# Performance work log

Measured on AMD Instinct MI355X. Metric: run time of the kernel, lower is better.

Reference implementation:

```python
import jax, jax.numpy as jnp
import numpy as np

B, S, D = 16, 8192, 256  # batch, seq_len, feature dim (== hdims)
HDIMS, HEADS = 256, 8
NEG_BIG = 1e12


def setup_inputs() -> dict:
    key = jax.random.key(0)
    k1, k2, k3 = jax.random.split(key, 3)
    x = jax.random.normal(k1, (B, S, D), dtype=jnp.float32)
    mask = jnp.ones((B, S), dtype=jnp.bool_)
    # glorot-ish scaling for stability
    k_kernel = jax.random.normal(k2, (D, HDIMS), dtype=jnp.float32) * (1.0 / np.sqrt(D))
    o_kernel = jax.random.normal(k3, (HDIMS, HEADS), dtype=jnp.float32) * (1.0 / np.sqrt(HDIMS))
    return {"x": x, "mask": mask, "k_kernel": k_kernel, "o_kernel": o_kernel}


def reference(x, mask, k_kernel, o_kernel):
    # scores: Dense(tanh) -> Dense(heads), shape (B, S, HEADS)
    w = jnp.tanh(x @ k_kernel) @ o_kernel
    m = mask.astype(jnp.float32)[..., None]            # (B, S, 1)
    w = w - (1.0 - m) * NEG_BIG
    w = jax.nn.softmax(w, axis=1)                      # softmax over sequence
    # fused weighted-sum pooling: avoids (B,S,H,D) broadcast intermediate
    pooled = jnp.einsum('bsh,bsd->bhd', w, x)          # (B, HEADS, D)
    return pooled.reshape(x.shape[0], HEADS * HDIMS)   # (B, HEADS*HDIMS)
```

## Files before the change

kernel.cpp:

```cpp
#include <hip/hip_runtime.h>

#define S_LEN 8192
#define DIM   256
#define CHUNK 512
#define TB    64
#define NIT   8
#define NBLK  256

typedef __attribute__((ext_vector_type(8))) short          short8;
typedef __attribute__((ext_vector_type(4))) unsigned short u16x4;
typedef __attribute__((ext_vector_type(4))) unsigned int   u32x4;
typedef __attribute__((ext_vector_type(4))) float          f32x4;
typedef __attribute__((ext_vector_type(8))) __bf16         bf16x8;

static __device__ __forceinline__ unsigned short f2bf(float f){
  return __builtin_bit_cast(unsigned short, (__bf16)f);
}
static __device__ __forceinline__ unsigned pk2bf(float lo, float hi){
  return (unsigned)f2bf(lo) | ((unsigned)f2bf(hi) << 16);
}
static __device__ __forceinline__ float bf2f(unsigned short h){
  unsigned int u = ((unsigned int)h) << 16;
  return __builtin_bit_cast(float, u);
}
static __device__ __forceinline__ float fast_tanh(float x){
  float e = __expf(2.0f * x);
  return 1.0f - 2.0f / (e + 1.0f);
}
static __device__ __forceinline__ f32x4 mfma_bf16(short8 a, short8 b, f32x4 c){
  return __builtin_amdgcn_mfma_f32_16x16x32_bf16(
      __builtin_bit_cast(bf16x8, a), __builtin_bit_cast(bf16x8, b), c, 0, 0, 0);
}
static __device__ __forceinline__ void softbar(){
  asm volatile("s_waitcnt lgkmcnt(0)\n\ts_barrier" ::: "memory");
}

__global__ void k_prep(const float* __restrict__ kk, unsigned short* __restrict__ KT){
  int idx = blockIdx.x * 512 + threadIdx.x;
  int n = idx >> 8, k = idx & 255;
  KT[(n << 8) + k] = f2bf(kk[(k << 8) + n]);
}


__global__ __launch_bounds__(512, 2) void k_main(
    const float* __restrict__ x, const int* __restrict__ mask,
    const float* __restrict__ ok, const unsigned short* __restrict__ KT,
    float* __restrict__ ACC, float* __restrict__ ML)
{
  __shared__ __align__(16) unsigned char sXB [32768];
  __shared__ __align__(16) unsigned char sXT2[65536];
  __shared__ __align__(16) unsigned char sT2 [32768];
  __shared__ __align__(16) unsigned char sOT [16*528];
  __shared__ __align__(16) unsigned char sPT [16*144];
  __shared__ float sWSum[4][16];
  __shared__ float sMaskB[CHUNK];

  const int tid = threadIdx.x;
  const int w   = tid >> 6;
  const int l   = tid & 63;
  const int l15 = l & 15;
  const int lhi = l >> 4;
  const int bid = blockIdx.x;
  const int b   = bid >> 4;
  const int chunk0 = (bid & 15) * CHUNK;

  for (int idx = tid; idx < 16 * 256; idx += 512){
    int h = idx >> 8, k = idx & 255;
    float v = (h < 8) ? ok[k * 8 + h] : 0.0f;
    *(unsigned short*)(sOT + h * 528 + k * 2) = f2bf(v);
  }
  sMaskB[tid] = mask[(size_t)b * S_LEN + chunk0 + tid] ? 0.0f : 1e12f;

  short8 aF[2][8];
  #pragma unroll
  for (int mi = 0; mi < 2; ++mi){
    int hidA = l15 + ((2*w + mi) << 4);
    #pragma unroll
    for (int k = 0; k < 8; ++k){
      int col = (k << 5) + (lhi << 3);
      aF[mi][k] = *(const short8*)((const unsigned char*)KT + (((size_t)hidA << 8) + col) * 2);
    }
  }

  const unsigned char* xb = (const unsigned char*)(x + ((size_t)b * S_LEN + chunk0) * DIM);
  const int dblk = l >> 2;

  f32x4 xr[8];
  #pragma unroll
  for (int q = 0; q < 8; ++q)
    xr[q] = *(const f32x4*)(xb + (((size_t)(8*w + q)) * DIM + 4*l) * 4);

  unsigned vd[8][2];
  #pragma unroll
  for (int q = 0; q < 8; ++q){
    vd[q][0] = pk2bf(xr[q][0], xr[q][1]);
    vd[q][1] = pk2bf(xr[q][2], xr[q][3]);
  }
  #pragma unroll
  for (int q = 0; q < 8; ++q){
    int r = 8*w + q;
    int srow = r ^ (dblk & 3);
    int off = ((l & 3) * 8) ^ (((srow >> 2) & 1) << 4);
    *(uint2*)(sXB + dblk * 2048 + srow * 32 + off) = make_uint2(vd[q][0], vd[q][1]);
  }
  #pragma unroll
  for (int i = 0; i < 4; ++i){
    int hh = i >> 1;
    unsigned dwv[4];
    #pragma unroll
    for (int j = 0; j < 4; ++j){
      unsigned a = vd[2*j][hh], c = vd[2*j+1][hh];
      dwv[j] = (i & 1) ? ((a >> 16) | (c & 0xFFFF0000u)) : ((a & 0xFFFFu) | (c << 16));
    }
    int d = 4*l + i;
    int key = ((d & 3) << 1) ^ ((d >> 2) & 7);
    *(u32x4*)(sXT2 + d * 128 + ((16*w) ^ (key << 4))) = (u32x4){dwv[0],dwv[1],dwv[2],dwv[3]};
  }
  #pragma unroll
  for (int q = 0; q < 8; ++q)
    xr[q] = *(const f32x4*)(xb + (((size_t)(TB + 8*w + q)) * DIM + 4*l) * 4);

  f32x4 acc3[2];
  acc3[0] = (f32x4){0.f,0.f,0.f,0.f};
  acc3[1] = acc3[0];
  float Lrun = 0.0f;

  __syncthreads();

  for (int it = 0; it < NIT; ++it){
    const int cur = it & 1;

    if (it + 1 < NIT){
      #pragma unroll
      for (int q = 0; q < 8; ++q){
        vd[q][0] = pk2bf(xr[q][0], xr[q][1]);
        vd[q][1] = pk2bf(xr[q][2], xr[q][3]);
      }
      unsigned char* dst = sXT2 + (cur ^ 1) * 32768;
      #pragma unroll
      for (int i = 0; i < 4; ++i){
        int hh = i >> 1;
        unsigned dwv[4];
        #pragma unroll
        for (int j = 0; j < 4; ++j){
          unsigned a = vd[2*j][hh], c = vd[2*j+1][hh];
          dwv[j] = (i & 1) ? ((a >> 16) | (c & 0xFFFF0000u)) : ((a & 0xFFFFu) | (c << 16));
        }
        int d = 4*l + i;
        int key = ((d & 3) << 1) ^ ((d >> 2) & 7);
        *(u32x4*)(dst + d * 128 + ((16*w) ^ (key << 4))) = (u32x4){dwv[0],dwv[1],dwv[2],dwv[3]};
      }
    }
    #pragma unroll
    for (int nt = 0; nt < 4; ++nt){
      int row = l15 + (nt << 4);
      f32x4 a0 = (f32x4){0.f,0.f,0.f,0.f};
      f32x4 a1 = a0;
      __builtin_amdgcn_s_setprio(1);
      #pragma unroll
      for (int k8 = 0; k8 < 8; ++k8){
        int dblkR = k8 * 2 + (lhi >> 1);
        int srowB = row ^ (dblkR & 3);
        int off = ((lhi & 1) * 16) ^ (((srowB >> 2) & 1) << 4);
        short8 bF = *(const short8*)(sXB + dblkR * 2048 + srowB * 32 + off);
        a0 = mfma_bf16(aF[0][k8], bF, a0);
        a1 = mfma_bf16(aF[1][k8], bF, a1);
      }
      __builtin_amdgcn_s_setprio(0);
      #pragma unroll
      for (int mi = 0; mi < 2; ++mi){
        f32x4 av = mi ? a1 : a0;
        u16x4 tv;
        #pragma unroll
        for (int r = 0; r < 4; ++r) tv[r] = f2bf(fast_tanh(av[r]));
        int hidb2 = ((((2*w + mi) << 4) + (lhi << 2))) * 2;
        *(u16x4*)(sT2 + row * 512 + (hidb2 ^ ((row & 7) << 4))) = tv;
      }
    }
    softbar();

    if (it + 1 < NIT){
      #pragma unroll
      for (int q = 0; q < 8; ++q){
        int r = 8*w + q;
        int srow = r ^ (dblk & 3);
        int off = ((l & 3) * 8) ^ (((srow >> 2) & 1) << 4);
        *(uint2*)(sXB + dblk * 2048 + srow * 32 + off) = make_uint2(vd[q][0], vd[q][1]);
      }
    }
    if (w < 4){
      int row = l15 + (w << 4);
      f32x4 a2 = (f32x4){0.f,0.f,0.f,0.f};
      __builtin_amdgcn_s_setprio(1);
      #pragma unroll
      for (int k = 0; k < 8; ++k){
        int col2 = (k << 6) + (lhi << 4);
        short8 aT = *(const short8*)(sT2 + row * 512 + (col2 ^ ((row & 7) << 4)));
        short8 bO = *(const short8*)(sOT + l15 * 528 + col2);
        a2 = mfma_bf16(aT, bO, a2);
      }
      __builtin_amdgcn_s_setprio(0);
      int rbase = (w << 4) + (lhi << 2);
      float psum = 0.0f;
      #pragma unroll
      for (int r = 0; r < 4; ++r){
        float p = __expf(a2[r] - sMaskB[it * TB + rbase + r]);
        unsigned short pb = f2bf(p);
        psum += bf2f(pb);
        *(unsigned short*)(sPT + l15 * 144 + (rbase + r) * 2) = pb;
      }
      psum += __shfl_xor(psum, 16);
      psum += __shfl_xor(psum, 32);
      Lrun += psum;
    }
    if (it + 2 < NIT){
      #pragma unroll
      for (int q = 0; q < 8; ++q)
        xr[q] = *(const f32x4*)(xb + (((size_t)((it+2)*TB + 8*w + q)) * DIM + 4*l) * 4);
    }
    softbar();

    {
      short8 aP0 = *(const short8*)(sPT + l15 * 144 + lhi * 16);
      short8 aP1 = *(const short8*)(sPT + l15 * 144 + 64 + lhi * 16);
      const unsigned char* srcX = sXT2 + cur * 32768;
      __builtin_amdgcn_s_setprio(1);
      #pragma unroll
      for (int mi = 0; mi < 2; ++mi){
        int d = (2*w + mi) * 16 + l15;
        int key = ((d & 3) << 1) ^ ((d >> 2) & 7);
        const unsigned char* pd = srcX + d * 128;
        short8 b0 = *(const short8*)(pd + (((     lhi * 16)) ^ (key << 4)));
        short8 b1 = *(const short8*)(pd + (((64 + lhi * 16)) ^ (key << 4)));
        acc3[mi] = mfma_bf16(aP0, b0, acc3[mi]);
        acc3[mi] = mfma_bf16(aP1, b1, acc3[mi]);
      }
      __builtin_amdgcn_s_setprio(0);
    }
    softbar();
  }

  if (lhi < 2){
    #pragma unroll
    for (int mi = 0; mi < 2; ++mi){
      int d = ((2*w + mi) << 4) + l15;
      #pragma unroll
      for (int r = 0; r < 4; ++r){
        int h = (lhi << 2) + r;
        ACC[((size_t)bid * 8 + h) * 256 + d] = acc3[mi][r];
      }
    }
  }
  if (w < 4 && l < 16) sWSum[w][l] = Lrun;
  __syncthreads();
  if (tid < 8)
    ML[bid * 8 + tid] = sWSum[0][tid] + sWSum[1][tid] + sWSum[2][tid] + sWSum[3][tid];
}

__global__ void k_merge(const float* __restrict__ ACC, const float* __restrict__ ML,
                        float* __restrict__ out){
  int b = blockIdx.x >> 3;
  int h = blockIdx.x & 7;
  int d = threadIdx.x;
  float L = 0.0f, V = 0.0f;
  #pragma unroll 4
  for (int c = 0; c < 16; ++c){
    int blk = b * 16 + c;
    L += ML[blk * 8 + h];
    V += ACC[((size_t)blk * 8 + h) * 256 + d];
  }
  out[(size_t)b * 2048 + h * 256 + d] = V / L;
}

extern "C" void kernel_launch(void* const* d_in, const int* in_sizes, int n_in,
                              void* d_out, int out_size, void* d_ws, size_t ws_size,
                              hipStream_t stream){
  const float* x   = (const float*)d_in[0];
  const int*  mask = (const int*) d_in[1];
  const float* kk  = (const float*)d_in[2];
  const float* ok  = (const float*)d_in[3];
  float* out = (float*)d_out;

  unsigned short* KT = (unsigned short*)d_ws;
  float* ACC = (float*)((char*)d_ws + 131072);
  float* ML  = (float*)((char*)d_ws + 131072 + 2097152);

  k_prep <<<128, 512, 0, stream>>>(kk, KT);
  k_main <<<NBLK, 512, 0, stream>>>(x, mask, ok, KT, ACC, ML);
  k_merge<<<128, 256, 0, stream>>>(ACC, ML, out);
}
```

Before: 58.23 us.

## Defer pooling MFMA to next iteration and double-buffer softmax weights to drop a barrier

The weighted-sum pooling step for chunk it is moved to the start of iteration it+1, with a final epilogue after the loop. The P tile is double-buffered so this shift is safe. This removes the third block-wide barrier per iteration and lets the pooling MFMAs overlap with the next chunk's projection work. It adds LDS for the second P buffer and changes when the x tile is converted and stored, which could affect occupancy and register pressure.

After: 56.96 us. 1.02x faster.

```diff
diff --git a/kernel.cpp b/kernel.cpp
--- a/kernel.cpp
+++ b/kernel.cpp
@@ -51,7 +51,7 @@
   __shared__ __align__(16) unsigned char sXT2[65536];
   __shared__ __align__(16) unsigned char sT2 [32768];
   __shared__ __align__(16) unsigned char sOT [16*528];
-  __shared__ __align__(16) unsigned char sPT [16*144];
+  __shared__ __align__(16) unsigned char sPT [2*2304];
   __shared__ float sWSum[4][16];
   __shared__ float sMaskB[CHUNK];
 
@@ -90,31 +90,33 @@
   for (int q = 0; q < 8; ++q)
     xr[q] = *(const f32x4*)(xb + (((size_t)(8*w + q)) * DIM + 4*l) * 4);
 
-  unsigned vd[8][2];
-  #pragma unroll
-  for (int q = 0; q < 8; ++q){
-    vd[q][0] = pk2bf(xr[q][0], xr[q][1]);
-    vd[q][1] = pk2bf(xr[q][2], xr[q][3]);
-  }
-  #pragma unroll
-  for (int q = 0; q < 8; ++q){
-    int r = 8*w + q;
-    int srow = r ^ (dblk & 3);
-    int off = ((l & 3) * 8) ^ (((srow >> 2) & 1) << 4);
-    *(uint2*)(sXB + dblk * 2048 + srow * 32 + off) = make_uint2(vd[q][0], vd[q][1]);
-  }
-  #pragma unroll
-  for (int i = 0; i < 4; ++i){
-    int hh = i >> 1;
-    unsigned dwv[4];
-    #pragma unroll
-    for (int j = 0; j < 4; ++j){
-      unsigned a = vd[2*j][hh], c = vd[2*j+1][hh];
-      dwv[j] = (i & 1) ? ((a >> 16) | (c & 0xFFFF0000u)) : ((a & 0xFFFFu) | (c << 16));
-    }
-    int d = 4*l + i;
-    int key = ((d & 3) << 1) ^ ((d >> 2) & 7);
-    *(u32x4*)(sXT2 + d * 128 + ((16*w) ^ (key << 4))) = (u32x4){dwv[0],dwv[1],dwv[2],dwv[3]};
+  {
+    unsigned vd[8][2];
+    #pragma unroll
+    for (int q = 0; q < 8; ++q){
+      vd[q][0] = pk2bf(xr[q][0], xr[q][1]);
+      vd[q][1] = pk2bf(xr[q][2], xr[q][3]);
+    }
+    #pragma unroll
+    for (int q = 0; q < 8; ++q){
+      int r = 8*w + q;
+      int srow = r ^ (dblk & 3);
+      int off = ((l & 3) * 8) ^ (((srow >> 2) & 1) << 4);
+      *(uint2*)(sXB + dblk * 2048 + srow * 32 + off) = make_uint2(vd[q][0], vd[q][1]);
+    }
+    #pragma unroll
+    for (int i = 0; i < 4; ++i){
+      int hh = i >> 1;
+      unsigned dwv[4];
+      #pragma unroll
+      for (int j = 0; j < 4; ++j){
+        unsigned a = vd[2*j][hh], c = vd[2*j+1][hh];
+        dwv[j] = (i & 1) ? ((a >> 16) | (c & 0xFFFF0000u)) : ((a & 0xFFFFu) | (c << 16));
+      }
+      int d = 4*l + i;
+      int key = ((d & 3) << 1) ^ ((d >> 2) & 7);
+      *(u32x4*)(sXT2 + d * 128 + ((16*w) ^ (key << 4))) = (u32x4){dwv[0],dwv[1],dwv[2],dwv[3]};
+    }
   }
   #pragma unroll
   for (int q = 0; q < 8; ++q)
@@ -128,15 +130,65 @@
   __syncthreads();
 
   for (int it = 0; it < NIT; ++it){
-    const int cur = it & 1;
+    if (it > 0){
+      const int pb = (it - 1) & 1;
+      short8 aP0 = *(const short8*)(sPT + pb * 2304 + l15 * 144 + lhi * 16);
+      short8 aP1 = *(const short8*)(sPT + pb * 2304 + l15 * 144 + 64 + lhi * 16);
+      const unsigned char* srcX = sXT2 + pb * 32768;
+      #pragma unroll
+      for (int mi = 0; mi < 2; ++mi){
+        int d = (2*w + mi) * 16 + l15;
+        int key = ((d & 3) << 1) ^ ((d >> 2) & 7);
+        const unsigned char* pd = srcX + d * 128;
+        short8 b0 = *(const short8*)(pd + (((     lhi * 16)) ^ (key << 4)));
+        short8 b1 = *(const short8*)(pd + (((64 + lhi * 16)) ^ (key << 4)));
+        acc3[mi] = mfma_bf16(aP0, b0, acc3[mi]);
+        acc3[mi] = mfma_bf16(aP1, b1, acc3[mi]);
+      }
+    }
+    #pragma unroll
+    for (int nt = 0; nt < 4; ++nt){
+      int row = l15 + (nt << 4);
+      f32x4 a0 = (f32x4){0.f,0.f,0.f,0.f};
+      f32x4 a1 = a0;
+      __builtin_amdgcn_s_setprio(1);
+      #pragma unroll
+      for (int k8 = 0; k8 < 8; ++k8){
+        int dblkR = k8 * 2 + (lhi >> 1);
+        int srowB = row ^ (dblkR & 3);
+        int off = ((lhi & 1) * 16) ^ (((srowB >> 2) & 1) << 4);
+        short8 bF = *(const short8*)(sXB + dblkR * 2048 + srowB * 32 + off);
+        a0 = mfma_bf16(aF[0][k8], bF, a0);
+        a1 = mfma_bf16(aF[1][k8], bF, a1);
+      }
+      __builtin_amdgcn_s_setprio(0);
+      #pragma unroll
+      for (int mi = 0; mi < 2; ++mi){
+        f32x4 av = mi ? a1 : a0;
+        u16x4 tv;
+        #pragma unroll
+        for (int r = 0; r < 4; ++r) tv[r] = f2bf(fast_tanh(av[r]));
+        int hidb2 = ((((2*w + mi) << 4) + (lhi << 2))) * 2;
+        *(u16x4*)(sT2 + row * 512 + (hidb2 ^ ((row & 7) << 4))) = tv;
+      }
+    }
+    softbar();
 
     if (it + 1 < NIT){
+      unsigned vd[8][2];
       #pragma unroll
       for (int q = 0; q < 8; ++q){
         vd[q][0] = pk2bf(xr[q][0], xr[q][1]);
         vd[q][1] = pk2bf(xr[q][2], xr[q][3]);
       }
-      unsigned char* dst = sXT2 + (cur ^ 1) * 32768;
+      #pragma unroll
+      for (int q = 0; q < 8; ++q){
+        int r = 8*w + q;
+        int srow = r ^ (dblk & 3);
+        int off = ((l & 3) * 8) ^ (((srow >> 2) & 1) << 4);
+        *(uint2*)(sXB + dblk * 2048 + srow * 32 + off) = make_uint2(vd[q][0], vd[q][1]);
+      }
+      unsigned char* dst = sXT2 + ((it + 1) & 1) * 32768;
       #pragma unroll
       for (int i = 0; i < 4; ++i){
         int hh = i >> 1;
@@ -151,43 +203,6 @@
         *(u32x4*)(dst + d * 128 + ((16*w) ^ (key << 4))) = (u32x4){dwv[0],dwv[1],dwv[2],dwv[3]};
       }
     }
-    #pragma unroll
-    for (int nt = 0; nt < 4; ++nt){
-      int row = l15 + (nt << 4);
-      f32x4 a0 = (f32x4){0.f,0.f,0.f,0.f};
-      f32x4 a1 = a0;
-      __builtin_amdgcn_s_setprio(1);
-      #pragma unroll
-      for (int k8 = 0; k8 < 8; ++k8){
-        int dblkR = k8 * 2 + (lhi >> 1);
-        int srowB = row ^ (dblkR & 3);
-        int off = ((lhi & 1) * 16) ^ (((srowB >> 2) & 1) << 4);
-        short8 bF = *(const short8*)(sXB + dblkR * 2048 + srowB * 32 + off);
-        a0 = mfma_bf16(aF[0][k8], bF, a0);
-        a1 = mfma_bf16(aF[1][k8], bF, a1);
-      }
-      __builtin_amdgcn_s_setprio(0);
-      #pragma unroll
-      for (int mi = 0; mi < 2; ++mi){
-        f32x4 av = mi ? a1 : a0;
-        u16x4 tv;
-        #pragma unroll
-        for (int r = 0; r < 4; ++r) tv[r] = f2bf(fast_tanh(av[r]));
-        int hidb2 = ((((2*w + mi) << 4) + (lhi << 2))) * 2;
-        *(u16x4*)(sT2 + row * 512 + (hidb2 ^ ((row & 7) << 4))) = tv;
-      }
-    }
-    softbar();
-
-    if (it + 1 < NIT){
-      #pragma unroll
-      for (int q = 0; q < 8; ++q){
-        int r = 8*w + q;
-        int srow = r ^ (dblk & 3);
-        int off = ((l & 3) * 8) ^ (((srow >> 2) & 1) << 4);
-        *(uint2*)(sXB + dblk * 2048 + srow * 32 + off) = make_uint2(vd[q][0], vd[q][1]);
-      }
-    }
     if (w < 4){
       int row = l15 + (w << 4);
       f32x4 a2 = (f32x4){0.f,0.f,0.f,0.f};
@@ -205,9 +220,9 @@
       #pragma unroll
       for (int r = 0; r < 4; ++r){
         float p = __expf(a2[r] - sMaskB[it * TB + rbase + r]);
-        unsigned short pb = f2bf(p);
-        psum += bf2f(pb);
-        *(unsigned short*)(sPT + l15 * 144 + (rbase + r) * 2) = pb;
+        unsigned short pb2 = f2bf(p);
+        psum += bf2f(pb2);
+        *(unsigned short*)(sPT + (it & 1) * 2304 + l15 * 144 + (rbase + r) * 2) = pb2;
       }
       psum += __shfl_xor(psum, 16);
       psum += __shfl_xor(psum, 32);
@@ -219,25 +234,23 @@
         xr[q] = *(const f32x4*)(xb + (((size_t)((it+2)*TB + 8*w + q)) * DIM + 4*l) * 4);
     }
     softbar();
-
-    {
-      short8 aP0 = *(const short8*)(sPT + l15 * 144 + lhi * 16);
-      short8 aP1 = *(const short8*)(sPT + l15 * 144 + 64 + lhi * 16);
-      const unsigned char* srcX = sXT2 + cur * 32768;
-      __builtin_amdgcn_s_setprio(1);
-      #pragma unroll
-      for (int mi = 0; mi < 2; ++mi){
-        int d = (2*w + mi) * 16 + l15;
-        int key = ((d & 3) << 1) ^ ((d >> 2) & 7);
-        const unsigned char* pd = srcX + d * 128;
-        short8 b0 = *(const short8*)(pd + (((     lhi * 16)) ^ (key << 4)));
-        short8 b1 = *(const short8*)(pd + (((64 + lhi * 16)) ^ (key << 4)));
-        acc3[mi] = mfma_bf16(aP0, b0, acc3[mi]);
-        acc3[mi] = mfma_bf16(aP1, b1, acc3[mi]);
-      }
-      __builtin_amdgcn_s_setprio(0);
-    }
-    softbar();
+  }
+
+  {
+    const int pb = (NIT - 1) & 1;
+    short8 aP0 = *(const short8*)(sPT + pb * 2304 + l15 * 144 + lhi * 16);
+    short8 aP1 = *(const short8*)(sPT + pb * 2304 + l15 * 144 + 64 + lhi * 16);
+    const unsigned char* srcX = sXT2 + pb * 32768;
+    #pragma unroll
+    for (int mi = 0; mi < 2; ++mi){
+      int d = (2*w + mi) * 16 + l15;
+      int key = ((d & 3) << 1) ^ ((d >> 2) & 7);
+      const unsigned char* pd = srcX + d * 128;
+      short8 b0 = *(const short8*)(pd + (((     lhi * 16)) ^ (key << 4)));
+      short8 b1 = *(const short8*)(pd + (((64 + lhi * 16)) ^ (key << 4)));
+      acc3[mi] = mfma_bf16(aP0, b0, acc3[mi]);
+      acc3[mi] = mfma_bf16(aP1, b1, acc3[mi]);
+    }
   }
 
   if (lhi < 2){
```

## Split fused score/pool kernel into separate scores and pooling kernels

Applied to the files above, without the earlier changes.

Splits the single fused kernel into a scores kernel, which writes bf16 softmax numerators to global memory, and a pooling kernel, which reads them back and does the weighted sum over x. Chunk size is halved and the block count doubled, each block requests higher occupancy, and shared memory per kernel drops. The cost is that x is read from HBM twice (about 134MB per pass) plus an extra kernel launch and a probabilities round-trip.

New measurement: 115.1 us. 1.98x slower.

```diff
diff --git a/kernel.cpp b/kernel.cpp
--- a/kernel.cpp
+++ b/kernel.cpp
@@ -2,10 +2,10 @@
 
 #define S_LEN 8192
 #define DIM   256
-#define CHUNK 512
+#define CHUNK 256
 #define TB    64
-#define NIT   8
-#define NBLK  256
+#define NIT   4
+#define NBLK  512
 
 typedef __attribute__((ext_vector_type(8))) short          short8;
 typedef __attribute__((ext_vector_type(4))) unsigned short u16x4;
@@ -41,17 +41,14 @@
   KT[(n << 8) + k] = f2bf(kk[(k << 8) + n]);
 }
 
-
-__global__ __launch_bounds__(512, 2) void k_main(
+__global__ __launch_bounds__(512, 4) void k_scores(
     const float* __restrict__ x, const int* __restrict__ mask,
     const float* __restrict__ ok, const unsigned short* __restrict__ KT,
-    float* __restrict__ ACC, float* __restrict__ ML)
+    unsigned short* __restrict__ Pt, float* __restrict__ Lp)
 {
-  __shared__ __align__(16) unsigned char sXB [32768];
-  __shared__ __align__(16) unsigned char sXT2[65536];
-  __shared__ __align__(16) unsigned char sT2 [32768];
-  __shared__ __align__(16) unsigned char sOT [16*528];
-  __shared__ __align__(16) unsigned char sPT [16*144];
+  __shared__ __align__(16) unsigned char sXB[32768];
+  __shared__ __align__(16) unsigned char sT2[32768];
+  __shared__ __align__(16) unsigned char sOT[8*528];
   __shared__ float sWSum[4][16];
   __shared__ float sMaskB[CHUNK];
 
@@ -61,15 +58,15 @@
   const int l15 = l & 15;
   const int lhi = l >> 4;
   const int bid = blockIdx.x;
-  const int b   = bid >> 4;
-  const int chunk0 = (bid & 15) * CHUNK;
-
-  for (int idx = tid; idx < 16 * 256; idx += 512){
+  const int b   = bid >> 5;
+  const int chunk0 = (bid & 31) * CHUNK;
+
+  for (int idx = tid; idx < 8 * 256; idx += 512){
     int h = idx >> 8, k = idx & 255;
-    float v = (h < 8) ? ok[k * 8 + h] : 0.0f;
-    *(unsigned short*)(sOT + h * 528 + k * 2) = f2bf(v);
-  }
-  sMaskB[tid] = mask[(size_t)b * S_LEN + chunk0 + tid] ? 0.0f : 1e12f;
+    *(unsigned short*)(sOT + h * 528 + k * 2) = f2bf(ok[k * 8 + h]);
+  }
+  if (tid < CHUNK)
+    sMaskB[tid] = mask[(size_t)b * S_LEN + chunk0 + tid] ? 0.0f : 1e12f;
 
   short8 aF[2][8];
   #pragma unroll
@@ -89,32 +86,161 @@
   #pragma unroll
   for (int q = 0; q < 8; ++q)
     xr[q] = *(const f32x4*)(xb + (((size_t)(8*w + q)) * DIM + 4*l) * 4);
-
-  unsigned vd[8][2];
-  #pragma unroll
-  for (int q = 0; q < 8; ++q){
-    vd[q][0] = pk2bf(xr[q][0], xr[q][1]);
-    vd[q][1] = pk2bf(xr[q][2], xr[q][3]);
-  }
-  #pragma unroll
-  for (int q = 0; q < 8; ++q){
-    int r = 8*w + q;
-    int srow = r ^ (dblk & 3);
-    int off = ((l & 3) * 8) ^ (((srow >> 2) & 1) << 4);
-    *(uint2*)(sXB + dblk * 2048 + srow * 32 + off) = make_uint2(vd[q][0], vd[q][1]);
-  }
-  #pragma unroll
-  for (int i = 0; i < 4; ++i){
-    int hh = i >> 1;
-    unsigned dwv[4];
-    #pragma unroll
-    for (int j = 0; j < 4; ++j){
-      unsigned a = vd[2*j][hh], c = vd[2*j+1][hh];
-      dwv[j] = (i & 1) ? ((a >> 16) | (c & 0xFFFF0000u)) : ((a & 0xFFFFu) | (c << 16));
-    }
-    int d = 4*l + i;
-    int key = ((d & 3) << 1) ^ ((d >> 2) & 7);
-    *(u32x4*)(sXT2 + d * 128 + ((16*w) ^ (key << 4))) = (u32x4){dwv[0],dwv[1],dwv[2],dwv[3]};
+  {
+    unsigned vd[8][2];
+    #pragma unroll
+    for (int q = 0; q < 8; ++q){
+      vd[q][0] = pk2bf(xr[q][0], xr[q][1]);
+      vd[q][1] = pk2bf(xr[q][2], xr[q][3]);
+    }
+    #pragma unroll
+    for (int q = 0; q < 8; ++q){
+      int r = 8*w + q;
+      int srow = r ^ (dblk & 3);
+      int off = ((l & 3) * 8) ^ (((srow >> 2) & 1) << 4);
+      *(uint2*)(sXB + dblk * 2048 + srow * 32 + off) = make_uint2(vd[q][0], vd[q][1]);
+    }
+  }
+  #pragma unroll
+  for (int q = 0; q < 8; ++q)
+    xr[q] = *(const f32x4*)(xb + (((size_t)(TB + 8*w + q)) * DIM + 4*l) * 4);
+
+  float Lrun = 0.0f;
+  __syncthreads();
+
+  for (int it = 0; it < NIT; ++it){
+    #pragma unroll
+    for (int nt = 0; nt < 4; ++nt){
+      int row = l15 + (nt << 4);
+      f32x4 a0 = (f32x4){0.f,0.f,0.f,0.f};
+      f32x4 a1 = a0;
+      __builtin_amdgcn_s_setprio(1);
+      #pragma unroll
+      for (int k8 = 0; k8 < 8; ++k8){
+        int dblkR = k8 * 2 + (lhi >> 1);
+        int srowB = row ^ (dblkR & 3);
+        int off = ((lhi & 1) * 16) ^ (((srowB >> 2) & 1) << 4);
+        short8 bF = *(const short8*)(sXB + dblkR * 2048 + srowB * 32 + off);
+        a0 = mfma_bf16(aF[0][k8], bF, a0);
+        a1 = mfma_bf16(aF[1][k8], bF, a1);
+      }
+      __builtin_amdgcn_s_setprio(0);
+      #pragma unroll
+      for (int mi = 0; mi < 2; ++mi){
+        f32x4 av = mi ? a1 : a0;
+        u16x4 tv;
+        #pragma unroll
+        for (int r = 0; r < 4; ++r) tv[r] = f2bf(fast_tanh(av[r]));
+        int hidb2 = ((((2*w + mi) << 4) + (lhi << 2))) * 2;
+        *(u16x4*)(sT2 + row * 512 + (hidb2 ^ ((row & 7) << 4))) = tv;
+      }
+    }
+    softbar();
+
+    if (it + 1 < NIT){
+      unsigned vd[8][2];
+      #pragma unroll
+      for (int q = 0; q < 8; ++q){
+        vd[q][0] = pk2bf(xr[q][0], xr[q][1]);
+        vd[q][1] = pk2bf(xr[q][2], xr[q][3]);
+      }
+      #pragma unroll
+      for (int q = 0; q < 8; ++q){
+        int r = 8*w + q;
+        int srow = r ^ (dblk & 3);
+        int off = ((l & 3) * 8) ^ (((srow >> 2) & 1) << 4);
+        *(uint2*)(sXB + dblk * 2048 + srow * 32 + off) = make_uint2(vd[q][0], vd[q][1]);
+      }
+    }
+    if (w < 4){
+      int row = l15 + (w << 4);
+      f32x4 a2 = (f32x4){0.f,0.f,0.f,0.f};
+      __builtin_amdgcn_s_setprio(1);
+      #pragma unroll
+      for (int k = 0; k < 8; ++k){
+        int col2 = (k << 6) + (lhi << 4);
+        short8 aT = *(const short8*)(sT2 + row * 512 + (col2 ^ ((row & 7) << 4)));
+        short8 bO = (l15 < 8) ? *(const short8*)(sOT + l15 * 528 + col2)
+                              : (short8){0,0,0,0,0,0,0,0};
+        a2 = mfma_bf16(aT, bO, a2);
+      }
+      __builtin_amdgcn_s_setprio(0);
+      int rbase = (w << 4) + (lhi << 2);
+      float psum = 0.0f;
+      u16x4 pv;
+      #pragma unroll
+      for (int r = 0; r < 4; ++r){
+        float p = __expf(a2[r] - sMaskB[it * TB + rbase + r]);
+        unsigned short pb2 = f2bf(p);
+        psum += bf2f(pb2);
+        pv[r] = pb2;
+      }
+      psum += __shfl_xor(psum, 16);
+      psum += __shfl_xor(psum, 32);
+      Lrun += psum;
+      if (l15 < 8){
+        int gt32 = ((bid & 31) << 3) + it * 2 + (w >> 1);
+        size_t off = ((size_t)b * 256 + gt32) * 512 + l15 * 64
+                   + (((w & 1) << 4) + (lhi << 2)) * 2;
+        *(u16x4*)((unsigned char*)Pt + off) = pv;
+      }
+    }
+    if (it + 2 < NIT){
+      #pragma unroll
+      for (int q = 0; q < 8; ++q)
+        xr[q] = *(const f32x4*)(xb + (((size_t)((it+2)*TB + 8*w + q)) * DIM + 4*l) * 4);
+    }
+    softbar();
+  }
+
+  if (w < 4 && l < 16) sWSum[w][l] = Lrun;
+  __syncthreads();
+  if (tid < 8)
+    Lp[bid * 8 + tid] = sWSum[0][tid] + sWSum[1][tid] + sWSum[2][tid] + sWSum[3][tid];
+}
+
+__global__ __launch_bounds__(512, 4) void k_pool(
+    const float* __restrict__ x, const unsigned short* __restrict__ Pt,
+    float* __restrict__ ACC)
+{
+  __shared__ __align__(16) unsigned char sXT2[65536];
+
+  const int tid = threadIdx.x;
+  const int w   = tid >> 6;
+  const int l   = tid & 63;
+  const int l15 = l & 15;
+  const int lhi = l >> 4;
+  const int bid = blockIdx.x;
+  const int b   = bid >> 5;
+  const int chunk0 = (bid & 31) * CHUNK;
+
+  const unsigned char* xb = (const unsigned char*)(x + ((size_t)b * S_LEN + chunk0) * DIM);
+  const unsigned char* PtB = (const unsigned char*)Pt;
+
+  f32x4 xr[8];
+  #pragma unroll
+  for (int q = 0; q < 8; ++q)
+    xr[q] = *(const f32x4*)(xb + (((size_t)(8*w + q)) * DIM + 4*l) * 4);
+  {
+    unsigned vd[8][2];
+    #pragma unroll
+    for (int q = 0; q < 8; ++q){
+      vd[q][0] = pk2bf(xr[q][0], xr[q][1]);
+      vd[q][1] = pk2bf(xr[q][2], xr[q][3]);
+    }
+    #pragma unroll
+    for (int i = 0; i < 4; ++i){
+      int hh = i >> 1;
+      unsigned dwv[4];
+      #pragma unroll
+      for (int j = 0; j < 4; ++j){
+        unsigned a = vd[2*j][hh], c = vd[2*j+1][hh];
+        dwv[j] = (i & 1) ? ((a >> 16) | (c & 0xFFFF0000u)) : ((a & 0xFFFFu) | (c << 16));
+      }
+      int d = 4*l + i;
+      int key = ((d & 3) << 1) ^ ((d >> 2) & 7);
+      *(u32x4*)(sXT2 + d * 128 + ((16*w) ^ (key << 4))) = (u32x4){dwv[0],dwv[1],dwv[2],dwv[3]};
+    }
   }
   #pragma unroll
   for (int q = 0; q < 8; ++q)
@@ -123,20 +249,35 @@
   f32x4 acc3[2];
   acc3[0] = (f32x4){0.f,0.f,0.f,0.f};
   acc3[1] = acc3[0];
-  float Lrun = 0.0f;
 
   __syncthreads();
 
   for (int it = 0; it < NIT; ++it){
-    const int cur = it & 1;
+    size_t tbase = ((size_t)b * 256 + ((bid & 31) << 3) + it * 2) * 512;
+    short8 aP0 = *(const short8*)(PtB + tbase +       l15 * 64 + lhi * 16);
+    short8 aP1 = *(const short8*)(PtB + tbase + 512 + l15 * 64 + lhi * 16);
+    const unsigned char* srcX = sXT2 + (it & 1) * 32768;
+    __builtin_amdgcn_s_setprio(1);
+    #pragma unroll
+    for (int mi = 0; mi < 2; ++mi){
+      int d = (2*w + mi) * 16 + l15;
+      int key = ((d & 3) << 1) ^ ((d >> 2) & 7);
+      const unsigned char* pd = srcX + d * 128;
+      short8 b0 = *(const short8*)(pd + (((     lhi * 16)) ^ (key << 4)));
+      short8 b1 = *(const short8*)(pd + (((64 + lhi * 16)) ^ (key << 4)));
+      acc3[mi] = mfma_bf16(aP0, b0, acc3[mi]);
+      acc3[mi] = mfma_bf16(aP1, b1, acc3[mi]);
+    }
+    __builtin_amdgcn_s_setprio(0);
 
     if (it + 1 < NIT){
+      unsigned vd[8][2];
       #pragma unroll
       for (int q = 0; q < 8; ++q){
         vd[q][0] = pk2bf(xr[q][0], xr[q][1]);
         vd[q][1] = pk2bf(xr[q][2], xr[q][3]);
       }
-      unsigned char* dst = sXT2 + (cur ^ 1) * 32768;
+      unsigned char* dst = sXT2 + ((it + 1) & 1) * 32768;
       #pragma unroll
       for (int i = 0; i < 4; ++i){
         int hh = i >> 1;
@@ -151,91 +292,10 @@
         *(u32x4*)(dst + d * 128 + ((16*w) ^ (key << 4))) = (u32x4){dwv[0],dwv[1],dwv[2],dwv[3]};
       }
     }
-    #pragma unroll
-    for (int nt = 0; nt < 4; ++nt){
-      int row = l15 + (nt << 4);
-      f32x4 a0 = (f32x4){0.f,0.f,0.f,0.f};
-      f32x4 a1 = a0;
-      __builtin_amdgcn_s_setprio(1);
-      #pragma unroll
-      for (int k8 = 0; k8 < 8; ++k8){
-        int dblkR = k8 * 2 + (lhi >> 1);
-        int srowB = row ^ (dblkR & 3);
-        int off = ((lhi & 1) * 16) ^ (((srowB >> 2) & 1) << 4);
-        short8 bF = *(const short8*)(sXB + dblkR * 2048 + srowB * 32 + off);
-        a0 = mfma_bf16(aF[0][k8], bF, a0);
-        a1 = mfma_bf16(aF[1][k8], bF, a1);
-      }
-      __builtin_amdgcn_s_setprio(0);
-      #pragma unroll
-      for (int mi = 0; mi < 2; ++mi){
-        f32x4 av = mi ? a1 : a0;
-        u16x4 tv;
-        #pragma unroll
-        for (int r = 0; r < 4; ++r) tv[r] = f2bf(fast_tanh(av[r]));
-        int hidb2 = ((((2*w + mi) << 4) + (lhi << 2))) * 2;
-        *(u16x4*)(sT2 + row * 512 + (hidb2 ^ ((row & 7) << 4))) = tv;
-      }
-    }
-    softbar();
-
-    if (it + 1 < NIT){
-      #pragma unroll
-      for (int q = 0; q < 8; ++q){
-        int r = 8*w + q;
-        int srow = r ^ (dblk & 3);
-        int off = ((l & 3) * 8) ^ (((srow >> 2) & 1) << 4);
-        *(uint2*)(sXB + dblk * 2048 + srow * 32 + off) = make_uint2(vd[q][0], vd[q][1]);
-      }
-    }
-    if (w < 4){
-      int row = l15 + (w << 4);
-      f32x4 a2 = (f32x4){0.f,0.f,0.f,0.f};
-      __builtin_amdgcn_s_setprio(1);
-      #pragma unroll
-      for (int k = 0; k < 8; ++k){
-        int col2 = (k << 6) + (lhi << 4);
-        short8 aT = *(const short8*)(sT2 + row * 512 + (col2 ^ ((row & 7) << 4)));
-        short8 bO = *(const short8*)(sOT + l15 * 528 + col2);
-        a2 = mfma_bf16(aT, bO, a2);
-      }
-      __builtin_amdgcn_s_setprio(0);
-      int rbase = (w << 4) + (lhi << 2);
-      float psum = 0.0f;
-      #pragma unroll
-      for (int r = 0; r < 4; ++r){
-        float p = __expf(a2[r] - sMaskB[it * TB + rbase + r]);
-        unsigned short pb = f2bf(p);
-        psum += bf2f(pb);
-        *(unsigned short*)(sPT + l15 * 144 + (rbase + r) * 2) = pb;
-      }
-      psum += __shfl_xor(psum, 16);
-      psum += __shfl_xor(psum, 32);
-      Lrun += psum;
-    }
     if (it + 2 < NIT){
       #pragma unroll
       for (int q = 0; q < 8; ++q)
         xr[q] = *(const f32x4*)(xb + (((size_t)((it+2)*TB + 8*w + q)) * DIM + 4*l) * 4);
-    }
-    softbar();
-
-    {
-      short8 aP0 = *(const short8*)(sPT + l15 * 144 + lhi * 16);
-      short8 aP1 = *(const short8*)(sPT + l15 * 144 + 64 + lhi * 16);
-      const unsigned char* srcX = sXT2 + cur * 32768;
-      __builtin_amdgcn_s_setprio(1);
-      #pragma unroll
-      for (int mi = 0; mi < 2; ++mi){
-        int d = (2*w + mi) * 16 + l15;
-        int key = ((d & 3) << 1) ^ ((d >> 2) & 7);
-        const unsigned char* pd = srcX + d * 128;
-        short8 b0 = *(const short8*)(pd + (((     lhi * 16)) ^ (key << 4)));
-        short8 b1 = *(const short8*)(pd + (((64 + lhi * 16)) ^ (key << 4)));
-        acc3[mi] = mfma_bf16(aP0, b0, acc3[mi]);
-        acc3[mi] = mfma_bf16(aP1, b1, acc3[mi]);
-      }
-      __builtin_amdgcn_s_setprio(0);
     }
     softbar();
   }
@@ -251,22 +311,18 @@
       }
     }
   }
-  if (w < 4 && l < 16) sWSum[w][l] = Lrun;
-  __syncthreads();
-  if (tid < 8)
-    ML[bid * 8 + tid] = sWSum[0][tid] + sWSum[1][tid] + sWSum[2][tid] + sWSum[3][tid];
-}
-
-__global__ void k_merge(const float* __restrict__ ACC, const float* __restrict__ ML,
+}
+
+__global__ void k_merge(const float* __restrict__ ACC, const float* __restrict__ Lp,
                         float* __restrict__ out){
   int b = blockIdx.x >> 3;
   int h = blockIdx.x & 7;
   int d = threadIdx.x;
   float L = 0.0f, V = 0.0f;
   #pragma unroll 4
-  for (int c = 0; c < 16; ++c){
-    int blk = b * 16 + c;
-    L += ML[blk * 8 + h];
+  for (int c = 0; c < 32; ++c){
+    int blk = (b << 5) + c;
+    L += Lp[blk * 8 + h];
     V += ACC[((size_t)blk * 8 + h) * 256 + d];
   }
   out[(size_t)b * 2048 + h * 256 + d] = V / L;
@@ -282,10 +338,12 @@
   float* out = (float*)d_out;
 
   unsigned short* KT = (unsigned short*)d_ws;
-  float* ACC = (float*)((char*)d_ws + 131072);
-  float* ML  = (float*)((char*)d_ws + 131072 + 2097152);
-
-  k_prep <<<128, 512, 0, stream>>>(kk, KT);
-  k_main <<<NBLK, 512, 0, stream>>>(x, mask, ok, KT, ACC, ML);
-  k_merge<<<128, 256, 0, stream>>>(ACC, ML, out);
-}
+  unsigned short* Pt = (unsigned short*)((char*)d_ws + 131072);
+  float* ACC = (float*)((char*)d_ws + 131072 + 2101248);
+  float* Lp  = (float*)((char*)d_ws + 131072 + 2101248 + 4194304);
+
+  k_prep  <<<128, 512, 0, stream>>>(kk, KT);
+  k_scores<<<NBLK, 512, 0, stream>>>(x, mask, ok, KT, Pt, Lp);
+  k_pool  <<<NBLK, 512, 0, stream>>>(x, Pt, ACC);
+  k_merge <<<128, 256, 0, stream>>>(ACC, Lp, out);
+}
```
